# Performance work log

Hardware: AMD Instinct MI355X
Metric: run time of the kernel (lower is better)

The kernel has to match this reference:

```python
import jax, jax.numpy as jnp
import numpy as np

N = 4096   # node_each_graph == in_feats (adjacency-row node features)
H = 512    # n_hidden
C = 2      # n_classes
E = 65536  # edges (avg degree 16)
NL = 5     # n_layers -> 4 GINConv layers
NR = NL - 2  # stacked hidden GIN layers (layers 1..3)


def _bn(x, g, b, m, v):
    # BatchNorm1d in eval mode (running stats), eps=1e-5
    return (x - m) * jax.lax.rsqrt(v + 1e-5) * g + b


def setup_inputs():
    key = jax.random.key(0)
    ks = iter(jax.random.split(key, 16))
    nk = lambda: next(ks)
    s = 0.02
    f32 = jnp.float32
    d = {}
    d["feat"] = jax.random.normal(nk(), (N, N), f32)
    d["edge_src"] = jax.random.randint(nk(), (E,), 0, N)
    d["edge_dst"] = jax.random.randint(nk(), (E,), 0, N)
    # GIN layer 0: MLP is Linear(N,H)-BN-ReLU-Linear(H,H); ApplyNodeFunc BN; outer BN
    d["eps0"] = jnp.zeros((), f32)
    d["W0a"] = jax.random.normal(nk(), (N, H), f32) * s
    d["b0a"] = jnp.zeros((H,), f32)
    d["W0b"] = jax.random.normal(nk(), (H, H), f32) * s
    d["b0b"] = jnp.zeros((H,), f32)
    for nm in ["bn0a", "bnA0", "bnO0"]:
        d[nm + "_g"] = jnp.ones((H,), f32); d[nm + "_b"] = jnp.zeros((H,), f32)
        d[nm + "_m"] = jnp.zeros((H,), f32); d[nm + "_v"] = jnp.ones((H,), f32)
    # GIN layers 1..NL-2 stacked (H -> H)
    d["epsR"] = jnp.zeros((NR,), f32)
    d["WRa"] = jax.random.normal(nk(), (NR, H, H), f32) * s
    d["bRa"] = jnp.zeros((NR, H), f32)
    d["WRb"] = jax.random.normal(nk(), (NR, H, H), f32) * s
    d["bRb"] = jnp.zeros((NR, H), f32)
    for nm in ["bnRa", "bnAR", "bnOR"]:
        d[nm + "_g"] = jnp.ones((NR, H), f32); d[nm + "_b"] = jnp.zeros((NR, H), f32)
        d[nm + "_m"] = jnp.zeros((NR, H), f32); d[nm + "_v"] = jnp.ones((NR, H), f32)
    # per-hidden-rep readout linears (batch_size = 1)
    d["Wp0"] = jax.random.normal(nk(), (N * N, C), f32) * 0.001
    d["bp0"] = jnp.zeros((C,), f32)
    d["WpR"] = jax.random.normal(nk(), (NL - 1, N * H, C), f32) * 0.001
    d["bpR"] = jnp.zeros((NL - 1, C), f32)
    return d


def _gin(h, src, dst, eps, Wa, ba, bna, Wb, bb, bnA, bnO):
    # GINConv sum-aggregation: (1+eps)*h + sum over in-neighbors
    agg = jax.ops.segment_sum(h[src], dst, num_segments=N)
    x = (1.0 + eps) * h + agg
    # MLP (num_layers=2): Linear -> BN -> ReLU -> Linear
    x = jax.nn.relu(_bn(x @ Wa + ba, *bna))
    x = x @ Wb + bb
    # ApplyNodeFunc: BN -> ReLU
    x = jax.nn.relu(_bn(x, *bnA))
    # Model-level BN -> ReLU
    x = jax.nn.relu(_bn(x, *bnO))
    return x


def reference(feat, edge_src, edge_dst, eps0, W0a, b0a, W0b, b0b,
              bn0a_g, bn0a_b, bn0a_m, bn0a_v, bnA0_g, bnA0_b, bnA0_m, bnA0_v,
              bnO0_g, bnO0_b, bnO0_m, bnO0_v,
              epsR, WRa, bRa, WRb, bRb,
              bnRa_g, bnRa_b, bnRa_m, bnRa_v, bnAR_g, bnAR_b, bnAR_m, bnAR_v,
              bnOR_g, bnOR_b, bnOR_m, bnOR_v, Wp0, bp0, WpR, bpR):
    h = _gin(feat, edge_src, edge_dst, eps0, W0a, b0a,
             (bn0a_g, bn0a_b, bn0a_m, bn0a_v), W0b, b0b,
             (bnA0_g, bnA0_b, bnA0_m, bnA0_v), (bnO0_g, bnO0_b, bnO0_m, bnO0_v))
    hs = [h]
    for i in range(NR):  # small fixed layer loop
        h = _gin(h, edge_src, edge_dst, epsR[i], WRa[i], bRa[i],
                 (bnRa_g[i], bnRa_b[i], bnRa_m[i], bnRa_v[i]), WRb[i], bRb[i],
                 (bnAR_g[i], bnAR_b[i], bnAR_m[i], bnAR_v[i]),
                 (bnOR_g[i], bnOR_b[i], bnOR_m[i], bnOR_v[i]))
        hs.append(h)
    # jumping-knowledge readout over hidden_rep (eval: dropout = identity)
    score = feat.reshape(1, -1) @ Wp0 + bp0
    for i, hi in enumerate(hs):
        score = score + hi.reshape(1, -1) @ WpR[i] + bpR[i]
    return score
```

## Files before the change

kernel.cpp:

```cpp
#include <hip/hip_runtime.h>
#include <cstdint>
#include <cstddef>

typedef __attribute__((ext_vector_type(8))) short short8;
typedef __attribute__((ext_vector_type(4))) float f32x4;
typedef __attribute__((ext_vector_type(4))) float f4;
typedef __attribute__((ext_vector_type(2))) float f2;
typedef __attribute__((ext_vector_type(4))) unsigned short us4;

#define NN 4096
#define HH 512
#define EE 65536

#define GLOAD(gp, lp) __builtin_amdgcn_global_load_lds( \
    (const __attribute__((address_space(1))) void*)(gp), \
    (__attribute__((address_space(3))) void*)(lp), 16, 0, 0)

__device__ __forceinline__ unsigned short f2bf(float x) {
    union { float f; unsigned u; } un; un.f = x;
    unsigned r = un.u + 0x7fffu + ((un.u >> 16) & 1u);
    return (unsigned short)(r >> 16);
}
__device__ __forceinline__ float b2f(unsigned short v) {
    union { unsigned u; float f; } un; un.u = ((unsigned)v) << 16; return un.f;
}

__global__ __launch_bounds__(256) void k_prep(const float* __restrict__ feat,
                                              const float* __restrict__ Wp0,
                                              unsigned short* __restrict__ featb,
                                              float* __restrict__ part,
                                              const float* __restrict__ W0a,
                                              const float* __restrict__ W0b,
                                              const float* __restrict__ WRa,
                                              const float* __restrict__ WRb,
                                              unsigned short* __restrict__ w0at,
                                              unsigned short* __restrict__ wt,
                                              const int* __restrict__ edst,
                                              int* __restrict__ starts,
                                              int* __restrict__ cursor) {
    __shared__ alignas(16) f4 fs[1024];
    __shared__ float s0[256], s1[256];
    __shared__ int wtot4[4], woff4[4];
    const int t = threadIdx.x;
    const int bid = blockIdx.x;
    if (bid == 0) {
        int* cnt = (int*)fs;
        for (int i = t; i < NN; i += 256) { cnt[i] = 0; cursor[i] = 0; }
        __syncthreads();
        const int4* e4 = (const int4*)edst;
        for (int b = 0; b < 64; b += 8) {
            int4 v[8];
#pragma unroll
            for (int k = 0; k < 8; ++k)
                v[k] = e4[(b + k) * 256 + t];
#pragma unroll
            for (int k = 0; k < 8; ++k) {
                atomicAdd(&cnt[v[k].x], 1); atomicAdd(&cnt[v[k].y], 1);
                atomicAdd(&cnt[v[k].z], 1); atomicAdd(&cnt[v[k].w], 1);
            }
        }
        __syncthreads();
        const int base = t * 16;
        int c[16]; int s = 0;
#pragma unroll
        for (int i = 0; i < 16; ++i) { c[i] = cnt[base + i]; s += c[i]; }
        const int lane = t & 63, wv = t >> 6;
        int inc = s;
        for (int d = 1; d < 64; d <<= 1) {
            int v = __shfl_up(inc, d);
            if (lane >= d) inc += v;
        }
        if (lane == 63) wtot4[wv] = inc;
        __syncthreads();
        if (t == 0) {
            int a = 0;
            for (int i = 0; i < 4; ++i) { woff4[i] = a; a += wtot4[i]; }
            starts[NN] = a;
        }
        __syncthreads();
        int run = woff4[wv] + inc - s;
#pragma unroll
        for (int i = 0; i < 16; ++i) { starts[base + i] = run; run += c[i]; }
    } else if (bid <= 4096) {
        const int b2 = bid - 1;
        const long B0 = (long)b2 * 1024;
        const f4* ff = (const f4*)feat;
        const f4* ww = (const f4*)Wp0;
        f4 v[4], wv[8];
#pragma unroll
        for (int k = 0; k < 4; ++k)
            v[k] = __builtin_nontemporal_load(ff + B0 + k * 256 + t);
#pragma unroll
        for (int k = 0; k < 8; ++k)
            wv[k] = __builtin_nontemporal_load(ww + 2 * B0 + k * 256 + t);
#pragma unroll
        for (int k = 0; k < 4; ++k) {
            fs[k * 256 + t] = v[k];
            us4 o;
            o.x = f2bf(v[k].x); o.y = f2bf(v[k].y); o.z = f2bf(v[k].z); o.w = f2bf(v[k].w);
            __builtin_nontemporal_store(o, (us4*)featb + B0 + k * 256 + t);
        }
        __syncthreads();
        float a0 = 0.f, a1 = 0.f;
#pragma unroll
        for (int k = 0; k < 8; ++k) {
            const int q = k * 256 + t;
            f2 fp = *(const f2*)((const char*)fs + (size_t)q * 8);
            a0 += fp.x * wv[k].x + fp.y * wv[k].z;
            a1 += fp.x * wv[k].y + fp.y * wv[k].w;
        }
        s0[t] = a0; s1[t] = a1;
        __syncthreads();
        for (int s = 128; s > 0; s >>= 1) {
            if (t < s) { s0[t] += s0[t + s]; s1[t] += s1[t + s]; }
            __syncthreads();
        }
        if (t == 0) { part[2 * b2] = s0[0]; part[2 * b2 + 1] = s1[0]; }
    } else {
        float (*tile)[33] = (float(*)[33])fs;
        const int tix = bid - 4097;
        const float* W; unsigned short* Wt; int K, kb, nb;
        if (tix < 2048) {
            W = W0a; Wt = w0at; K = NN; kb = tix >> 4; nb = tix & 15;
        } else {
            const int t2 = tix - 2048;
            const int z = t2 >> 8, r = t2 & 255;
            W = (z == 0) ? W0b : (z < 4) ? WRa + (size_t)(z - 1) * HH * HH
                                         : WRb + (size_t)(z - 4) * HH * HH;
            Wt = wt + (size_t)z * HH * HH; K = HH; kb = r >> 4; nb = r & 15;
        }
        const int k0 = kb * 32, n0 = nb * 32;
        const int tx = t & 31, ty = t >> 5;
        for (int r = ty; r < 32; r += 8)
            tile[r][tx] = W[(size_t)(k0 + r) * HH + n0 + tx];
        __syncthreads();
        for (int r = ty; r < 32; r += 8)
            Wt[(size_t)(n0 + r) * K + k0 + tx] = f2bf(tile[tx][r]);
    }
}

__global__ __launch_bounds__(256) void k_gemm0s(
    const unsigned short* __restrict__ A, const unsigned short* __restrict__ Bt,
    float* __restrict__ outf,
    const int* __restrict__ esrc, const int* __restrict__ edst,
    const int* __restrict__ starts, int* __restrict__ cursor, int* __restrict__ sorted)
{
    constexpr int K = NN, N = HH;
    __shared__ alignas(16) unsigned short As[2 * 8192];
    __shared__ alignas(16) unsigned short Bs[2 * 8192];
    const int bid = blockIdx.x;
    const int t = threadIdx.x;
    if (bid >= 512) {
        const int e = (bid - 512) * 256 + t;
        const int d = edst[e];
        const int p = starts[d] + atomicAdd(&cursor[d], 1);
        sorted[p] = esrc[e];
        return;
    }
    const int bx = bid & 31, by = (bid >> 5) & 3, bz = bid >> 7;
    const int lane = t & 63, w = t >> 6;
    const int wr = w >> 1, wc = w & 1;
    const int l15 = lane & 15, l4 = lane >> 4;
    const int m0 = bx * 128, n0 = by * 128;
    const int kbase = bz * (K / 4);

    f32x4 acc[4][4];
#pragma unroll
    for (int i = 0; i < 4; ++i)
#pragma unroll
        for (int j = 0; j < 4; ++j) acc[i][j] = (f32x4){0.f, 0.f, 0.f, 0.f};

    const int ar = t >> 3;
    const int ac = (t & 7) ^ (ar & 7);
    const unsigned short* ga = A + (size_t)(m0 + ar) * K + kbase + ac * 8;
    const unsigned short* gb = Bt + (size_t)(n0 + ar) * K + kbase + ac * 8;

    auto stage = [&](int kt, int buf) {
        const int ko = kt * 64;
        unsigned short* Ad = As + buf * 8192 + t * 8;
        unsigned short* Bd = Bs + buf * 8192 + t * 8;
        GLOAD(ga + ko, Ad);
        GLOAD(ga + (size_t)32 * K + ko, Ad + 2048);
        GLOAD(ga + (size_t)64 * K + ko, Ad + 4096);
        GLOAD(ga + (size_t)96 * K + ko, Ad + 6144);
        GLOAD(gb + ko, Bd);
        GLOAD(gb + (size_t)32 * K + ko, Bd + 2048);
        GLOAD(gb + (size_t)64 * K + ko, Bd + 4096);
        GLOAD(gb + (size_t)96 * K + ko, Bd + 6144);
    };

    const int rsw = l15 & 7;
    const int nk = (K / 4) >> 6;
    stage(0, 0);
    __syncthreads();
    for (int kt = 0; kt < nk; ++kt) {
        const int cur = kt & 1;
        if (kt + 1 < nk) stage(kt + 1, cur ^ 1);
        const unsigned short* Ac = As + cur * 8192;
        const unsigned short* Bc = Bs + cur * 8192;
        short8 aF[4][2], bF[4][2];
#pragma unroll
        for (int i = 0; i < 4; ++i)
#pragma unroll
            for (int ks = 0; ks < 2; ++ks)
                aF[i][ks] = *(const short8*)(Ac + (wr * 64 + i * 16 + l15) * 64
                                                + (((ks * 4 + l4) ^ rsw) * 8));
#pragma unroll
        for (int j = 0; j < 4; ++j)
#pragma unroll
            for (int ks = 0; ks < 2; ++ks)
                bF[j][ks] = *(const short8*)(Bc + (wc * 64 + j * 16 + l15) * 64
                                                + (((ks * 4 + l4) ^ rsw) * 8));
#pragma unroll
        for (int ks = 0; ks < 2; ++ks)
#pragma unroll
            for (int i = 0; i < 4; ++i)
#pragma unroll
                for (int j = 0; j < 4; ++j)
                    acc[i][j] = __builtin_amdgcn_mfma_f32_16x16x32_bf16(aF[i][ks], bF[j][ks], acc[i][j], 0, 0, 0);
        __syncthreads();
    }

    float* op = outf + (size_t)bz * NN * N;
    const int mrow = m0 + wr * 64;
#pragma unroll
    for (int j = 0; j < 4; ++j) {
        const int cg = n0 + wc * 64 + j * 16 + l15;
#pragma unroll
        for (int i = 0; i < 4; ++i)
#pragma unroll
            for (int r = 0; r < 4; ++r)
                __builtin_nontemporal_store(acc[i][j][r],
                    op + (size_t)(mrow + i * 16 + l4 * 4 + r) * N + cg);
    }
}

#define SORTCAP 6144
__global__ __launch_bounds__(256) void k_redsortb(const float* __restrict__ p,
                                                  unsigned short* __restrict__ G0b,
                                                  const int* __restrict__ starts,
                                                  int* __restrict__ a) {
    __shared__ int buf[SORTCAP];
    const int bid = blockIdx.x;
    const int t = threadIdx.x;
    if (bid >= 2048) {
        const int binbase = (bid - 2048) * 256;
        const int lo = starts[binbase], hi = starts[binbase + 256];
        const int n = hi - lo;
        if (n <= SORTCAP) {
            for (int i = t; i < n; i += 256) buf[i] = a[lo + i];
            __syncthreads();
            const int d = binbase + t;
            const int s = starts[d] - lo, e = starts[d + 1] - lo;
            for (int i = s + 1; i < e; ++i) {
                int v = buf[i]; int j = i - 1;
                while (j >= s && buf[j] > v) { buf[j + 1] = buf[j]; --j; }
                buf[j + 1] = v;
            }
            __syncthreads();
            for (int i = t; i < n; i += 256) a[lo + i] = buf[i];
        } else {
            const int d = binbase + t;
            const int s = starts[d], e = starts[d + 1];
            for (int i = s + 1; i < e; ++i) {
                int v = a[i]; int j = i - 1;
                while (j >= s && a[j] > v) { a[j + 1] = a[j]; --j; }
                a[j + 1] = v;
            }
        }
        return;
    }
    const long S = (long)NN * HH / 4;
    long i = bid * 256L + t;
    const f4* pp = (const f4*)p;
    f4 x = __builtin_nontemporal_load(pp + i);
    f4 y = __builtin_nontemporal_load(pp + i + S);
    f4 c = __builtin_nontemporal_load(pp + i + 2 * S);
    f4 d4 = __builtin_nontemporal_load(pp + i + 3 * S);
    us4 o;
    o.x = f2bf((x.x + y.x) + (c.x + d4.x));
    o.y = f2bf((x.y + y.y) + (c.y + d4.y));
    o.z = f2bf((x.z + y.z) + (c.z + d4.z));
    o.w = f2bf((x.w + y.w) + (c.w + d4.w));
    ((us4*)G0b)[i] = o;
}

template<int EPI, bool DOT, bool STOREH>
__global__ __launch_bounds__(256) void k_gemmH(
    const unsigned short* __restrict__ A, const unsigned short* __restrict__ Bt,
    const float* __restrict__ bias,
    const float* __restrict__ g1, const float* __restrict__ b1,
    const float* __restrict__ m1, const float* __restrict__ v1,
    const float* __restrict__ g2, const float* __restrict__ b2,
    const float* __restrict__ m2, const float* __restrict__ v2,
    unsigned short* __restrict__ outb,
    const float* __restrict__ wq, float* __restrict__ part, int slotbase)
{
    constexpr int K = HH, N = HH;
    __shared__ alignas(16) unsigned short As[2 * 8192];
    __shared__ alignas(16) unsigned short Bs[2 * 4096];
    const int t = threadIdx.x;
    const int lane = t & 63, w = t >> 6;
    const int wr = w >> 1, wc = w & 1;
    const int l15 = lane & 15, l4 = lane >> 4;
    const int m0 = blockIdx.x * 128, n0 = blockIdx.y * 64;

    f32x4 acc[4][2];
#pragma unroll
    for (int i = 0; i < 4; ++i)
#pragma unroll
        for (int j = 0; j < 2; ++j) acc[i][j] = (f32x4){0.f, 0.f, 0.f, 0.f};

    const int ar = t >> 3;
    const int ac = (t & 7) ^ (ar & 7);
    const unsigned short* ga = A + (size_t)(m0 + ar) * K + ac * 8;
    const unsigned short* gb = Bt + (size_t)(n0 + ar) * K + ac * 8;

    auto stage = [&](int kt, int buf) {
        const int ko = kt * 64;
        unsigned short* Ad = As + buf * 8192 + t * 8;
        unsigned short* Bd = Bs + buf * 4096 + t * 8;
        GLOAD(ga + ko, Ad);
        GLOAD(ga + (size_t)32 * K + ko, Ad + 2048);
        GLOAD(ga + (size_t)64 * K + ko, Ad + 4096);
        GLOAD(ga + (size_t)96 * K + ko, Ad + 6144);
        GLOAD(gb + ko, Bd);
        GLOAD(gb + (size_t)32 * K + ko, Bd + 2048);
    };

    const int rsw = l15 & 7;
    const int nk = K >> 6;
    stage(0, 0);
    __syncthreads();
    for (int kt = 0; kt < nk; ++kt) {
        const int cur = kt & 1;
        if (kt + 1 < nk) stage(kt + 1, cur ^ 1);
        const unsigned short* Ac = As + cur * 8192;
        const unsigned short* Bc = Bs + cur * 4096;
        short8 aF[4][2], bF[2][2];
#pragma unroll
        for (int i = 0; i < 4; ++i)
#pragma unroll
            for (int ks = 0; ks < 2; ++ks)
                aF[i][ks] = *(const short8*)(Ac + (wr * 64 + i * 16 + l15) * 64
                                                + (((ks * 4 + l4) ^ rsw) * 8));
#pragma unroll
        for (int j = 0; j < 2; ++j)
#pragma unroll
            for (int ks = 0; ks < 2; ++ks)
                bF[j][ks] = *(const short8*)(Bc + (wc * 32 + j * 16 + l15) * 64
                                                + (((ks * 4 + l4) ^ rsw) * 8));
#pragma unroll
        for (int ks = 0; ks < 2; ++ks)
#pragma unroll
            for (int i = 0; i < 4; ++i)
#pragma unroll
                for (int j = 0; j < 2; ++j)
                    acc[i][j] = __builtin_amdgcn_mfma_f32_16x16x32_bf16(aF[i][ks], bF[j][ks], acc[i][j], 0, 0, 0);
        __syncthreads();
    }

    const int mrow = m0 + wr * 64;
    float d0 = 0.f, d1 = 0.f;
#pragma unroll
    for (int j = 0; j < 2; ++j) {
        const int cg = n0 + wc * 32 + j * 16 + l15;
        const float bi = bias[cg];
        const float sc1 = rsqrtf(v1[cg] + 1e-5f) * g1[cg];
        const float sh1 = b1[cg] - m1[cg] * sc1;
        float sc2 = 1.f, sh2 = 0.f;
        if (EPI == 3) {
            sc2 = rsqrtf(v2[cg] + 1e-5f) * g2[cg];
            sh2 = b2[cg] - m2[cg] * sc2;
        }
#pragma unroll
        for (int i = 0; i < 4; ++i) {
#pragma unroll
            for (int r = 0; r < 4; ++r) {
                const int rg = mrow + i * 16 + l4 * 4 + r;
                float x = acc[i][j][r];
                x = fmaxf((x + bi) * sc1 + sh1, 0.f);
                if (EPI == 3) x = fmaxf(x * sc2 + sh2, 0.f);
                if constexpr (STOREH) outb[(size_t)rg * N + cg] = f2bf(x);
                if constexpr (DOT) {
                    f2 wvv = __builtin_nontemporal_load((const f2*)wq + (size_t)rg * N + cg);
                    d0 += x * wvv.x; d1 += x * wvv.y;
                }
            }
        }
    }
    if constexpr (DOT) {
        float* r0 = (float*)As;
        float* r1 = r0 + 256;
        __syncthreads();
        r0[t] = d0; r1[t] = d1;
        __syncthreads();
        for (int s = 128; s > 0; s >>= 1) {
            if (t < s) { r0[t] += r0[t + s]; r1[t] += r1[t + s]; }
            __syncthreads();
        }
        if (t == 0) {
            const int slot = slotbase + blockIdx.y * gridDim.x + blockIdx.x;
            part[2 * slot] = r0[0]; part[2 * slot + 1] = r1[0];
        }
    }
}

__global__ __launch_bounds__(128) void k_agg0(
    const unsigned short* __restrict__ G0, const int* __restrict__ starts,
    const int* __restrict__ sorted, const float* __restrict__ epsp,
    const float* __restrict__ bias,
    const float* __restrict__ bg, const float* __restrict__ bb,
    const float* __restrict__ bm, const float* __restrict__ bv,
    unsigned short* __restrict__ outb)
{
    const int d = blockIdx.x, t = threadIdx.x;
    const float ep = 1.0f + epsp[0];
    ushort4 ow = ((const ushort4*)(G0 + (size_t)d * HH))[t];
    float sx = 0.f, sy = 0.f, sz = 0.f, sw = 0.f;
    const int e0 = starts[d], e1 = starts[d + 1];
    int i = e0;
    for (; i + 8 <= e1; i += 8) {
        ushort4 x[8];
#pragma unroll
        for (int k = 0; k < 8; ++k)
            x[k] = ((const ushort4*)(G0 + (size_t)sorted[i + k] * HH))[t];
#pragma unroll
        for (int k = 0; k < 8; ++k) {
            sx += b2f(x[k].x); sy += b2f(x[k].y); sz += b2f(x[k].z); sw += b2f(x[k].w);
        }
    }
    for (; i < e1; ++i) {
        ushort4 x = ((const ushort4*)(G0 + (size_t)sorted[i] * HH))[t];
        sx += b2f(x.x); sy += b2f(x.y); sz += b2f(x.z); sw += b2f(x.w);
    }
    float4 bi = ((const float4*)bias)[t];
    float4 g4 = ((const float4*)bg)[t];
    float4 b4 = ((const float4*)bb)[t];
    float4 m4 = ((const float4*)bm)[t];
    float4 v4 = ((const float4*)bv)[t];
    float x0 = ep * b2f(ow.x) + sx + bi.x;
    float x1 = ep * b2f(ow.y) + sy + bi.y;
    float x2 = ep * b2f(ow.z) + sz + bi.z;
    float x3 = ep * b2f(ow.w) + sw + bi.w;
    x0 = fmaxf((x0 - m4.x) * rsqrtf(v4.x + 1e-5f) * g4.x + b4.x, 0.f);
    x1 = fmaxf((x1 - m4.y) * rsqrtf(v4.y + 1e-5f) * g4.y + b4.y, 0.f);
    x2 = fmaxf((x2 - m4.z) * rsqrtf(v4.z + 1e-5f) * g4.z + b4.z, 0.f);
    x3 = fmaxf((x3 - m4.w) * rsqrtf(v4.w + 1e-5f) * g4.w + b4.w, 0.f);
    ushort4 o; o.x = f2bf(x0); o.y = f2bf(x1); o.z = f2bf(x2); o.w = f2bf(x3);
    ((ushort4*)(outb + (size_t)d * HH))[t] = o;
}

__global__ __launch_bounds__(128) void k_aggL(
    const unsigned short* __restrict__ hsrc, const int* __restrict__ starts,
    const int* __restrict__ sorted, const float* __restrict__ epsp,
    unsigned short* __restrict__ outb)
{
    const int d = blockIdx.x, t = threadIdx.x;
    const float ep = 1.0f + epsp[0];
    ushort4 ow = ((const ushort4*)(hsrc + (size_t)d * HH))[t];
    float sx = 0.f, sy = 0.f, sz = 0.f, sw = 0.f;
    const int e0 = starts[d], e1 = starts[d + 1];
    int i = e0;
    for (; i + 8 <= e1; i += 8) {
        ushort4 x[8];
#pragma unroll
        for (int k = 0; k < 8; ++k)
            x[k] = ((const ushort4*)(hsrc + (size_t)sorted[i + k] * HH))[t];
#pragma unroll
        for (int k = 0; k < 8; ++k) {
            sx += b2f(x[k].x); sy += b2f(x[k].y); sz += b2f(x[k].z); sw += b2f(x[k].w);
        }
    }
    for (; i < e1; ++i) {
        ushort4 x = ((const ushort4*)(hsrc + (size_t)sorted[i] * HH))[t];
        sx += b2f(x.x); sy += b2f(x.y); sz += b2f(x.z); sw += b2f(x.w);
    }
    ushort4 o;
    o.x = f2bf(ep * b2f(ow.x) + sx);
    o.y = f2bf(ep * b2f(ow.y) + sy);
    o.z = f2bf(ep * b2f(ow.z) + sz);
    o.w = f2bf(ep * b2f(ow.w) + sw);
    ((ushort4*)(outb + (size_t)d * HH))[t] = o;
}

__global__ __launch_bounds__(256) void k_final(const float* __restrict__ part, int nslot,
                                               const float* __restrict__ bp0, const float* __restrict__ bpR,
                                               float* __restrict__ out) {
    __shared__ float s0[256], s1[256];
    int t = threadIdx.x;
    float a0 = 0.f, a1 = 0.f;
    for (int i = t; i < nslot; i += 256) { a0 += part[2 * i]; a1 += part[2 * i + 1]; }
    s0[t] = a0; s1[t] = a1;
    __syncthreads();
    for (int s = 128; s > 0; s >>= 1) {
        if (t < s) { s0[t] += s0[t + s]; s1[t] += s1[t + s]; }
        __syncthreads();
    }
    if (t == 0) {
        out[0] = s0[0] + bp0[0] + bpR[0] + bpR[2] + bpR[4] + bpR[6];
        out[1] = s1[0] + bp0[1] + bpR[1] + bpR[3] + bpR[5] + bpR[7];
    }
}

extern "C" void kernel_launch(void* const* d_in, const int* in_sizes, int n_in,
                              void* d_out, int out_size, void* d_ws, size_t ws_size,
                              hipStream_t stream)
{
    const float* feat = (const float*)d_in[0];
    const int*   esrc = (const int*)d_in[1];
    const int*   edst = (const int*)d_in[2];
    const float* eps0 = (const float*)d_in[3];
    const float* W0a  = (const float*)d_in[4];
    const float* b0a  = (const float*)d_in[5];
    const float* W0b  = (const float*)d_in[6];
    const float* b0b  = (const float*)d_in[7];
    const float* bn0a_g = (const float*)d_in[8];
    const float* bn0a_b = (const float*)d_in[9];
    const float* bn0a_m = (const float*)d_in[10];
    const float* bn0a_v = (const float*)d_in[11];
    const float* bnA0_g = (const float*)d_in[12];
    const float* bnA0_b = (const float*)d_in[13];
    const float* bnA0_m = (const float*)d_in[14];
    const float* bnA0_v = (const float*)d_in[15];
    const float* bnO0_g = (const float*)d_in[16];
    const float* bnO0_b = (const float*)d_in[17];
    const float* bnO0_m = (const float*)d_in[18];
    const float* bnO0_v = (const float*)d_in[19];
    const float* epsR = (const float*)d_in[20];
    const float* WRa  = (const float*)d_in[21];
    const float* bRa  = (const float*)d_in[22];
    const float* WRb  = (const float*)d_in[23];
    const float* bRb  = (const float*)d_in[24];
    const float* bnRa_g = (const float*)d_in[25];
    const float* bnRa_b = (const float*)d_in[26];
    const float* bnRa_m = (const float*)d_in[27];
    const float* bnRa_v = (const float*)d_in[28];
    const float* bnAR_g = (const float*)d_in[29];
    const float* bnAR_b = (const float*)d_in[30];
    const float* bnAR_m = (const float*)d_in[31];
    const float* bnAR_v = (const float*)d_in[32];
    const float* bnOR_g = (const float*)d_in[33];
    const float* bnOR_b = (const float*)d_in[34];
    const float* bnOR_m = (const float*)d_in[35];
    const float* bnOR_v = (const float*)d_in[36];
    const float* Wp0 = (const float*)d_in[37];
    const float* bp0 = (const float*)d_in[38];
    const float* WpR = (const float*)d_in[39];
    const float* bpR = (const float*)d_in[40];
    float* out = (float*)d_out;

    char* ws = (char*)d_ws;
    const size_t MB = 1024 * 1024;
    int*   starts = (int*)(ws + 0x10000);
    int*   cursor = (int*)(ws + 0x20000);
    int*   sorted = (int*)(ws + 0x30000);
    float* part   = (float*)(ws + 0x70000);
    unsigned short* featb = (unsigned short*)(ws + 1 * MB);
    unsigned short* w0at  = (unsigned short*)(ws + 33 * MB);
    unsigned short* wt    = (unsigned short*)(ws + 37 * MB);
    unsigned short* G0b   = (unsigned short*)(ws + 41 * MB);
    unsigned short* xb = (unsigned short*)(ws + 49 * MB);
    unsigned short* yb = (unsigned short*)(ws + 53 * MB);
    unsigned short* hb = (unsigned short*)(ws + 57 * MB);
    float* pbuf = (float*)(ws + 57 * MB);

    k_prep<<<1 + 4096 + 3840, 256, 0, stream>>>(feat, Wp0, featb, part,
                                                W0a, W0b, WRa, WRb, w0at, wt,
                                                edst, starts, cursor);

    k_gemm0s<<<768, 256, 0, stream>>>(featb, w0at, pbuf, esrc, edst, starts, cursor, sorted);

    k_redsortb<<<2064, 256, 0, stream>>>(pbuf, G0b, starts, sorted);

    k_agg0<<<NN, 128, 0, stream>>>(G0b, starts, sorted, eps0, b0a,
                                   bn0a_g, bn0a_b, bn0a_m, bn0a_v, xb);

    const dim3 hg(32, 8);
    k_gemmH<3, true, true><<<hg, 256, 0, stream>>>(xb, wt,
        b0b, bnA0_g, bnA0_b, bnA0_m, bnA0_v, bnO0_g, bnO0_b, bnO0_m, bnO0_v,
        hb, WpR, part, 4096);

    for (int i = 0; i < 3; ++i) {
        const unsigned short* hp = hb + (size_t)i * NN * HH;
        unsigned short* hn = hb + (size_t)(i + 1) * NN * HH;
        k_aggL<<<NN, 128, 0, stream>>>(hp, starts, sorted, epsR + i, xb);
        k_gemmH<1, false, true><<<hg, 256, 0, stream>>>(xb, wt + (size_t)(1 + i) * HH * HH,
            bRa + (size_t)i * HH,
            bnRa_g + (size_t)i * HH, bnRa_b + (size_t)i * HH, bnRa_m + (size_t)i * HH, bnRa_v + (size_t)i * HH,
            nullptr, nullptr, nullptr, nullptr,
            yb, nullptr, nullptr, 0);
        if (i < 2) {
            k_gemmH<3, true, true><<<hg, 256, 0, stream>>>(yb, wt + (size_t)(4 + i) * HH * HH,
                bRb + (size_t)i * HH,
                bnAR_g + (size_t)i * HH, bnAR_b + (size_t)i * HH, bnAR_m + (size_t)i * HH, bnAR_v + (size_t)i * HH,
                bnOR_g + (size_t)i * HH, bnOR_b + (size_t)i * HH, bnOR_m + (size_t)i * HH, bnOR_v + (size_t)i * HH,
                hn, WpR + (size_t)(i + 1) * NN * HH * 2, part, 4096 + (i + 1) * 256);
        } else {
            k_gemmH<3, true, false><<<hg, 256, 0, stream>>>(yb, wt + (size_t)(4 + i) * HH * HH,
                bRb + (size_t)i * HH,
                bnAR_g + (size_t)i * HH, bnAR_b + (size_t)i * HH, bnAR_m + (size_t)i * HH, bnAR_v + (size_t)i * HH,
                bnOR_g + (size_t)i * HH, bnOR_b + (size_t)i * HH, bnOR_m + (size_t)i * HH, bnOR_v + (size_t)i * HH,
                nullptr, WpR + (size_t)(i + 1) * NN * HH * 2, part, 4096 + (i + 1) * 256);
        }
    }

    k_final<<<1, 256, 0, stream>>>(part, 4096 + 4 * 256, bp0, bpR, out);
}
```

Baseline: 243.0 us.

## Move feat·Wp0 readout dot product from prep kernel into gemm0 kernel using bf16 feat

The readout dot product of feat with Wp0 moves out of the prep kernel and into extra blocks of the first GEMM kernel. Those blocks read the bf16 copy of feat instead of the fp32 original and each block covers 2048 elements. This reduces the number of partial sums from 4096 to 1024, and the partial-buffer offsets are shifted to match. The prep kernel becomes a pure conversion with no LDS reduction and no Wp0 traffic, and the Wp0 stream now runs alongside the GEMM blocks. In exchange, the readout now sees bf16-rounded features, which costs some precision.

```diff
diff --git a/kernel.cpp b/kernel.cpp
--- a/kernel.cpp
+++ b/kernel.cpp
@@ -26,9 +26,7 @@
 }
 
 __global__ __launch_bounds__(256) void k_prep(const float* __restrict__ feat,
-                                              const float* __restrict__ Wp0,
                                               unsigned short* __restrict__ featb,
-                                              float* __restrict__ part,
                                               const float* __restrict__ W0a,
                                               const float* __restrict__ W0b,
                                               const float* __restrict__ WRa,
@@ -38,13 +36,11 @@
                                               const int* __restrict__ edst,
                                               int* __restrict__ starts,
                                               int* __restrict__ cursor) {
-    __shared__ alignas(16) f4 fs[1024];
-    __shared__ float s0[256], s1[256];
+    __shared__ alignas(16) int cnt[NN];
     __shared__ int wtot4[4], woff4[4];
     const int t = threadIdx.x;
     const int bid = blockIdx.x;
     if (bid == 0) {
-        int* cnt = (int*)fs;
         for (int i = t; i < NN; i += 256) { cnt[i] = 0; cursor[i] = 0; }
         __syncthreads();
         const int4* e4 = (const int4*)edst;
@@ -85,39 +81,18 @@
         const int b2 = bid - 1;
         const long B0 = (long)b2 * 1024;
         const f4* ff = (const f4*)feat;
-        const f4* ww = (const f4*)Wp0;
-        f4 v[4], wv[8];
+        f4 v[4];
 #pragma unroll
         for (int k = 0; k < 4; ++k)
             v[k] = __builtin_nontemporal_load(ff + B0 + k * 256 + t);
 #pragma unroll
-        for (int k = 0; k < 8; ++k)
-            wv[k] = __builtin_nontemporal_load(ww + 2 * B0 + k * 256 + t);
-#pragma unroll
         for (int k = 0; k < 4; ++k) {
-            fs[k * 256 + t] = v[k];
             us4 o;
             o.x = f2bf(v[k].x); o.y = f2bf(v[k].y); o.z = f2bf(v[k].z); o.w = f2bf(v[k].w);
             __builtin_nontemporal_store(o, (us4*)featb + B0 + k * 256 + t);
         }
-        __syncthreads();
-        float a0 = 0.f, a1 = 0.f;
-#pragma unroll
-        for (int k = 0; k < 8; ++k) {
-            const int q = k * 256 + t;
-            f2 fp = *(const f2*)((const char*)fs + (size_t)q * 8);
-            a0 += fp.x * wv[k].x + fp.y * wv[k].z;
-            a1 += fp.x * wv[k].y + fp.y * wv[k].w;
-        }
-        s0[t] = a0; s1[t] = a1;
-        __syncthreads();
-        for (int s = 128; s > 0; s >>= 1) {
-            if (t < s) { s0[t] += s0[t + s]; s1[t] += s1[t + s]; }
-            __syncthreads();
-        }
-        if (t == 0) { part[2 * b2] = s0[0]; part[2 * b2 + 1] = s1[0]; }
     } else {
-        float (*tile)[33] = (float(*)[33])fs;
+        float (*tile)[33] = (float(*)[33])cnt;
         const int tix = bid - 4097;
         const float* W; unsigned short* Wt; int K, kb, nb;
         if (tix < 2048) {
@@ -143,13 +118,48 @@
     const unsigned short* __restrict__ A, const unsigned short* __restrict__ Bt,
     float* __restrict__ outf,
     const int* __restrict__ esrc, const int* __restrict__ edst,
-    const int* __restrict__ starts, int* __restrict__ cursor, int* __restrict__ sorted)
+    const int* __restrict__ starts, int* __restrict__ cursor, int* __restrict__ sorted,
+    const float* __restrict__ Wp0, float* __restrict__ part)
 {
     constexpr int K = NN, N = HH;
     __shared__ alignas(16) unsigned short As[2 * 8192];
     __shared__ alignas(16) unsigned short Bs[2 * 8192];
     const int bid = blockIdx.x;
     const int t = threadIdx.x;
+    if (bid >= 768) {
+        const int db = bid - 768;
+        const long c0 = (long)db * 2048;
+        const short8* fb = (const short8*)A;
+        const f4* wp = (const f4*)Wp0;
+        float a0 = 0.f, a1 = 0.f;
+#pragma unroll
+        for (int k = 0; k < 8; ++k) {
+            const long ci = c0 + k * 256 + t;
+            short8 fv = fb[ci];
+            f4 w0 = __builtin_nontemporal_load(wp + ci * 4);
+            f4 w1 = __builtin_nontemporal_load(wp + ci * 4 + 1);
+            f4 w2 = __builtin_nontemporal_load(wp + ci * 4 + 2);
+            f4 w3 = __builtin_nontemporal_load(wp + ci * 4 + 3);
+            float f0 = b2f((unsigned short)fv[0]), f1 = b2f((unsigned short)fv[1]);
+            float f2v = b2f((unsigned short)fv[2]), f3 = b2f((unsigned short)fv[3]);
+            float f4v = b2f((unsigned short)fv[4]), f5 = b2f((unsigned short)fv[5]);
+            float f6 = b2f((unsigned short)fv[6]), f7 = b2f((unsigned short)fv[7]);
+            a0 += f0 * w0.x + f1 * w0.z + f2v * w1.x + f3 * w1.z
+                + f4v * w2.x + f5 * w2.z + f6 * w3.x + f7 * w3.z;
+            a1 += f0 * w0.y + f1 * w0.w + f2v * w1.y + f3 * w1.w
+                + f4v * w2.y + f5 * w2.w + f6 * w3.y + f7 * w3.w;
+        }
+        float* r0 = (float*)As;
+        float* r1 = r0 + 256;
+        r0[t] = a0; r1[t] = a1;
+        __syncthreads();
+        for (int s = 128; s > 0; s >>= 1) {
+            if (t < s) { r0[t] += r0[t + s]; r1[t] += r1[t + s]; }
+            __syncthreads();
+        }
+        if (t == 0) { part[2 * db] = r0[0]; part[2 * db + 1] = r1[0]; }
+        return;
+    }
     if (bid >= 512) {
         const int e = (bid - 512) * 256 + t;
         const int d = edst[e];
@@ -565,11 +575,12 @@
     unsigned short* hb = (unsigned short*)(ws + 57 * MB);
     float* pbuf = (float*)(ws + 57 * MB);
 
-    k_prep<<<1 + 4096 + 3840, 256, 0, stream>>>(feat, Wp0, featb, part,
+    k_prep<<<1 + 4096 + 3840, 256, 0, stream>>>(feat, featb,
                                                 W0a, W0b, WRa, WRb, w0at, wt,
                                                 edst, starts, cursor);
 
-    k_gemm0s<<<768, 256, 0, stream>>>(featb, w0at, pbuf, esrc, edst, starts, cursor, sorted);
+    k_gemm0s<<<1792, 256, 0, stream>>>(featb, w0at, pbuf, esrc, edst, starts, cursor, sorted,
+                                       Wp0, part);
 
     k_redsortb<<<2064, 256, 0, stream>>>(pbuf, G0b, starts, sorted);
 
@@ -579,7 +590,7 @@
     const dim3 hg(32, 8);
     k_gemmH<3, true, true><<<hg, 256, 0, stream>>>(xb, wt,
         b0b, bnA0_g, bnA0_b, bnA0_m, bnA0_v, bnO0_g, bnO0_b, bnO0_m, bnO0_v,
-        hb, WpR, part, 4096);
+        hb, WpR, part, 1024);
 
     for (int i = 0; i < 3; ++i) {
         const unsigned short* hp = hb + (size_t)i * NN * HH;
@@ -595,15 +606,15 @@
                 bRb + (size_t)i * HH,
                 bnAR_g + (size_t)i * HH, bnAR_b + (size_t)i * HH, bnAR_m + (size_t)i * HH, bnAR_v + (size_t)i * HH,
                 bnOR_g + (size_t)i * HH, bnOR_b + (size_t)i * HH, bnOR_m + (size_t)i * HH, bnOR_v + (size_t)i * HH,
-                hn, WpR + (size_t)(i + 1) * NN * HH * 2, part, 4096 + (i + 1) * 256);
+                hn, WpR + (size_t)(i + 1) * NN * HH * 2, part, 1024 + (i + 1) * 256);
         } else {
             k_gemmH<3, true, false><<<hg, 256, 0, stream>>>(yb, wt + (size_t)(4 + i) * HH * HH,
                 bRb + (size_t)i * HH,
                 bnAR_g + (size_t)i * HH, bnAR_b + (size_t)i * HH, bnAR_m + (size_t)i * HH, bnAR_v + (size_t)i * HH,
                 bnOR_g + (size_t)i * HH, bnOR_b + (size_t)i * HH, bnOR_m + (size_t)i * HH, bnOR_v + (size_t)i * HH,
-                nullptr, WpR + (size_t)(i + 1) * NN * HH * 2, part, 4096 + (i + 1) * 256);
-        }
-    }
-
-    k_final<<<1, 256, 0, stream>>>(part, 4096 + 4 * 256, bp0, bpR, out);
-}
+                nullptr, WpR + (size_t)(i + 1) * NN * HH * 2, part, 1024 + (i + 1) * 256);
+        }
+    }
+
+    k_final<<<1, 256, 0, stream>>>(part, 2048, bp0, bpR, out);
+}
```

Measured after the change: 260.3 us. +7.1%, slower.
